# Optimization experiments

Hardware: AMD Instinct MI355X
Metric: run time of the kernel (lower is better)

Reference implementation:

```python
import jax, jax.numpy as jnp
import numpy as np

N_NODES = 50000
N_EDGES = 500000
ATOM_DIM = 128
BOND_DIM = 64
EMB = 128
N_GRAPHS = 256
NUM_LAYER = 2


def _kaiming_uniform(key, fan_out, fan_in):
    # kaiming_uniform_ with nonlinearity='relu': bound = sqrt(6 / fan_in) * sqrt(2)/1 adjustments
    gain = np.sqrt(2.0)
    bound = gain * np.sqrt(3.0 / fan_in)
    return jax.random.uniform(key, (fan_out, fan_in), jnp.float32, -bound, bound)


def setup_inputs() -> dict:
    key = jax.random.key(0)
    ks = jax.random.split(key, 12)
    x = jax.random.normal(ks[0], (N_NODES, ATOM_DIM), jnp.float32)
    edge_attr = jax.random.normal(ks[1], (N_EDGES, BOND_DIM), jnp.float32)
    edge_index = jax.random.randint(ks[2], (2, N_EDGES), 0, N_NODES, jnp.int64)
    batch = jnp.sort(jax.random.randint(ks[3], (N_NODES,), 0, N_GRAPHS, jnp.int64))
    Wa = _kaiming_uniform(ks[4], EMB, ATOM_DIM)
    ba = jnp.zeros((EMB,), jnp.float32)
    Wb = _kaiming_uniform(ks[5], EMB, BOND_DIM)
    bb = jnp.zeros((EMB,), jnp.float32)
    W1 = _kaiming_uniform(ks[6], EMB, EMB)
    b1 = jnp.zeros((EMB,), jnp.float32)
    W2 = _kaiming_uniform(ks[7], EMB // 2, EMB)
    b2 = jnp.zeros((EMB // 2,), jnp.float32)
    W3 = _kaiming_uniform(ks[8], 1, EMB // 2)
    return {"x": x, "edge_attr": edge_attr, "edge_index": edge_index, "batch": batch,
            "Wa": Wa, "ba": ba, "Wb": Wb, "bb": bb,
            "W1": W1, "b1": b1, "W2": W2, "b2": b2, "W3": W3}


def reference(x, edge_attr, edge_index, batch, Wa, ba, Wb, bb, W1, b1, W2, b2, W3):
    src, dst = edge_index[0], edge_index[1]
    # Step 1: embeddings
    node_emb = x @ Wa.T + ba          # [N, EMB]
    edge_emb = edge_attr @ Wb.T + bb  # [E, EMB]
    # Step 2: message passing layers: gather, multiply with edge_emb, scatter-add, residual
    for _ in range(NUM_LAYER):
        msg = node_emb[src] * edge_emb                           # [E, EMB]
        agg = jax.ops.segment_sum(msg, dst, num_segments=N_NODES)  # [N, EMB]
        node_emb = node_emb + agg
    # Step 3: energy MLP (ReLU first, per nn.Sequential)
    h = jax.nn.relu(node_emb)
    h = jax.nn.relu(h @ W1.T + b1)
    h = jax.nn.relu(h @ W2.T + b2)
    node_energy = h @ W3.T            # [N, 1], no bias
    # Step 4: global add pool over graphs
    dg = jax.ops.segment_sum(node_energy, batch, num_segments=N_GRAPHS)  # [G, 1]
    return dg
```

## Files before the change

kernel.cpp:

```cpp
#include <hip/hip_runtime.h>
#include <cstdio>
#include <cstdint>

#define N_NODES 50000
#define N_EDGES 500000
#define EMB 128
#define BOND 64
#define NGRAPH 256
#define NB_SCAN ((N_NODES + 255) / 256)
#define NSTRIP (N_NODES / 16)
#define HSTR 136

typedef short bf16x8 __attribute__((ext_vector_type(8)));
typedef float f32x4  __attribute__((ext_vector_type(4)));

__device__ __forceinline__ unsigned short f2bf(float v){
  unsigned u = __float_as_uint(v);
  unsigned r = (u + 0x7fffu + ((u >> 16) & 1u)) >> 16;
  return (unsigned short)r;
}
__device__ __forceinline__ float bf2f(unsigned short u){
  return __uint_as_float(((unsigned)u) << 16);
}

__global__ void prep_w(const float* __restrict__ Wa, const float* __restrict__ W1,
                       const float* __restrict__ W2, unsigned short* __restrict__ wabf,
                       unsigned short* __restrict__ w1bf, unsigned short* __restrict__ w2bf)
{
  int i = blockIdx.x * 256 + threadIdx.x;
  int i2 = i & 16383;
  int j = i2 & 7, lb = (i2 >> 3) & 63, kc = (i2 >> 9) & 3, tn = i2 >> 11;
  int lm = lb & 15, q = lb >> 4;
  int row = tn * 16 + lm, col = kc * 32 + q * 8 + j;
  if (i < 16384){
    wabf[i] = f2bf(Wa[row * EMB + col]);
  } else if (i < 32768){
    w1bf[i2] = f2bf(W1[row * EMB + col]);
  } else if (i < 32768 + 8192){
    w2bf[i2] = f2bf(W2[row * EMB + col]);
  }
}

__global__ __launch_bounds__(256) void node_gemm_mfma(const float* __restrict__ x,
    const unsigned short* __restrict__ wabf, const float* __restrict__ ba,
    float* __restrict__ out)
{
  const int t = threadIdx.x;
  const int wv = t >> 6, l = t & 63;
  const int lm = l & 15, q = l >> 4;
  union U8 { bf16x8 v; unsigned short s[8]; };
  const int strip = blockIdx.x * 4 + wv;
  if (strip >= NSTRIP) return;
  const long n0 = (long)strip * 16;

  bf16x8 a[4];
  #pragma unroll
  for (int kc = 0; kc < 4; kc++){
    const float* ap = x + (n0 + lm) * (long)EMB + kc * 32 + q * 8;
    float4 x0 = *(const float4*)ap;
    float4 x1 = *(const float4*)(ap + 4);
    U8 u;
    u.s[0] = f2bf(x0.x); u.s[1] = f2bf(x0.y); u.s[2] = f2bf(x0.z); u.s[3] = f2bf(x0.w);
    u.s[4] = f2bf(x1.x); u.s[5] = f2bf(x1.y); u.s[6] = f2bf(x1.z); u.s[7] = f2bf(x1.w);
    a[kc] = u.v;
  }
  float biasv[8];
  #pragma unroll
  for (int tn = 0; tn < 8; tn++) biasv[tn] = ba[tn * 16 + lm];

  #pragma unroll
  for (int tn = 0; tn < 8; tn++){
    f32x4 acc = {0.f, 0.f, 0.f, 0.f};
    #pragma unroll
    for (int kc = 0; kc < 4; kc++){
      bf16x8 bf = *(const bf16x8*)(wabf + (size_t)((tn * 4 + kc) * 64 + l) * 8);
      acc = __builtin_amdgcn_mfma_f32_16x16x32_bf16(a[kc], bf, acc, 0, 0, 0);
    }
    #pragma unroll
    for (int i = 0; i < 4; i++)
      out[(n0 + q * 4 + i) * (long)EMB + tn * 16 + lm] = acc[i] + biasv[tn];
  }
}

__global__ __launch_bounds__(256) void edge_gemm_mfma(
    const float* __restrict__ attr, const float* __restrict__ Wb,
    const float* __restrict__ bb, const int* __restrict__ cedge,
    unsigned short* __restrict__ eemb)
{
  __shared__ unsigned short hs[4][32 * HSTR];
  const int t = threadIdx.x;
  const int wv = t >> 6;
  const int l  = t & 63;
  const int lm = l & 15;
  const int q  = l >> 4;
  union U8 { bf16x8 v; unsigned short s[8]; };

  bf16x8 bfrag[8][2];
  float bias[8];
  #pragma unroll
  for (int tn = 0; tn < 8; tn++){
    bias[tn] = bb[tn * 16 + lm];
    #pragma unroll
    for (int h = 0; h < 2; h++){
      const float* wp = Wb + (tn * 16 + lm) * BOND + h * 32 + q * 8;
      float4 w0 = *(const float4*)wp;
      float4 w1 = *(const float4*)(wp + 4);
      U8 u;
      u.s[0] = f2bf(w0.x); u.s[1] = f2bf(w0.y); u.s[2] = f2bf(w0.z); u.s[3] = f2bf(w0.w);
      u.s[4] = f2bf(w1.x); u.s[5] = f2bf(w1.y); u.s[6] = f2bf(w1.z); u.s[7] = f2bf(w1.w);
      bfrag[tn][h] = u.v;
    }
  }

  unsigned short* hw = hs[wv];
  const long stride = (long)gridDim.x * 4 * 32;
  for (long p0 = ((long)blockIdx.x * 4 + wv) * 32; p0 < N_EDGES; p0 += stride){
    long eidA = (long)cedge[p0 + lm];
    long eidB = (long)cedge[p0 + 16 + lm];
    bf16x8 afA[2], afB[2];
    #pragma unroll
    for (int h = 0; h < 2; h++){
      const float* apA = attr + eidA * BOND + h * 32 + q * 8;
      const float* apB = attr + eidB * BOND + h * 32 + q * 8;
      float4 a0 = *(const float4*)apA;
      float4 a1 = *(const float4*)(apA + 4);
      float4 b0 = *(const float4*)apB;
      float4 b1 = *(const float4*)(apB + 4);
      U8 u;
      u.s[0] = f2bf(a0.x); u.s[1] = f2bf(a0.y); u.s[2] = f2bf(a0.z); u.s[3] = f2bf(a0.w);
      u.s[4] = f2bf(a1.x); u.s[5] = f2bf(a1.y); u.s[6] = f2bf(a1.z); u.s[7] = f2bf(a1.w);
      afA[h] = u.v;
      u.s[0] = f2bf(b0.x); u.s[1] = f2bf(b0.y); u.s[2] = f2bf(b0.z); u.s[3] = f2bf(b0.w);
      u.s[4] = f2bf(b1.x); u.s[5] = f2bf(b1.y); u.s[6] = f2bf(b1.z); u.s[7] = f2bf(b1.w);
      afB[h] = u.v;
    }
    #pragma unroll
    for (int tn = 0; tn < 8; tn++){
      f32x4 accA = {0.f, 0.f, 0.f, 0.f};
      f32x4 accB = {0.f, 0.f, 0.f, 0.f};
      accA = __builtin_amdgcn_mfma_f32_16x16x32_bf16(afA[0], bfrag[tn][0], accA, 0, 0, 0);
      accA = __builtin_amdgcn_mfma_f32_16x16x32_bf16(afA[1], bfrag[tn][1], accA, 0, 0, 0);
      accB = __builtin_amdgcn_mfma_f32_16x16x32_bf16(afB[0], bfrag[tn][0], accB, 0, 0, 0);
      accB = __builtin_amdgcn_mfma_f32_16x16x32_bf16(afB[1], bfrag[tn][1], accB, 0, 0, 0);
      #pragma unroll
      for (int i = 0; i < 4; i++){
        hw[(q * 4 + i) * HSTR + tn * 16 + lm]        = f2bf(accA[i] + bias[tn]);
        hw[(16 + q * 4 + i) * HSTR + tn * 16 + lm]   = f2bf(accB[i] + bias[tn]);
      }
    }
    #pragma unroll
    for (int rb = 0; rb < 8; rb++){
      int row = rb * 4 + q;
      ushort4 v0 = *(const ushort4*)(hw + row * HSTR + lm * 8);
      ushort4 v1 = *(const ushort4*)(hw + row * HSTR + lm * 8 + 4);
      unsigned short* op = eemb + (p0 + row) * (long)EMB + lm * 8;
      *(ushort4*)op = v0;
      *(ushort4*)(op + 4) = v1;
    }
  }
}


__global__ __launch_bounds__(256) void count_deg(const int* __restrict__ ei,
                                                 int* __restrict__ deg)
{
  int e = blockIdx.x * 256 + threadIdx.x;
  if (e < N_EDGES) atomicAdd(&deg[ei[N_EDGES + e]], 1);
}

__global__ __launch_bounds__(256) void scan_s1(const int* __restrict__ deg,
                                               int* __restrict__ blocksum)
{
  int i = blockIdx.x * 256 + threadIdx.x;
  int lane = threadIdx.x & 63, w = threadIdx.x >> 6;
  int v = (i < N_NODES) ? deg[i] : 0;
  #pragma unroll
  for (int o = 32; o > 0; o >>= 1) v += __shfl_down(v, o, 64);
  __shared__ int ws4[4];
  if (lane == 0) ws4[w] = v;
  __syncthreads();
  if (threadIdx.x == 0) blocksum[blockIdx.x] = ws4[0] + ws4[1] + ws4[2] + ws4[3];
}

__global__ __launch_bounds__(256) void scan_s2(const int* __restrict__ blocksum,
                                               int* __restrict__ blockoff,
                                               int* __restrict__ off)
{
  int t = threadIdx.x;
  int lane = t & 63, w = t >> 6;
  int v = (t < NB_SCAN) ? blocksum[t] : 0;
  int x = v;
  #pragma unroll
  for (int d = 1; d < 64; d <<= 1){
    int y = __shfl_up(x, d, 64);
    if (lane >= d) x += y;
  }
  __shared__ int wsum[4];
  if (lane == 63) wsum[w] = x;
  __syncthreads();
  int wo = 0;
  for (int j = 0; j < w; j++) wo += wsum[j];
  if (t < NB_SCAN) blockoff[t] = wo + x - v;
  if (t == 0) off[N_NODES] = wsum[0] + wsum[1] + wsum[2] + wsum[3];
}

__global__ __launch_bounds__(256) void scan_s3(const int* __restrict__ deg,
    const int* __restrict__ blockoff, int* __restrict__ off, int* __restrict__ fill)
{
  int i = blockIdx.x * 256 + threadIdx.x;
  int lane = threadIdx.x & 63, w = threadIdx.x >> 6;
  int v = (i < N_NODES) ? deg[i] : 0;
  int x = v;
  #pragma unroll
  for (int d = 1; d < 64; d <<= 1){
    int y = __shfl_up(x, d, 64);
    if (lane >= d) x += y;
  }
  __shared__ int wsum[4];
  if (lane == 63) wsum[w] = x;
  __syncthreads();
  int wo = 0;
  for (int j = 0; j < w; j++) wo += wsum[j];
  if (i < N_NODES){
    int excl = blockoff[blockIdx.x] + wo + x - v;
    off[i] = excl;
    fill[i] = excl;
  }
}

__global__ __launch_bounds__(256) void scatter_edges(const int* __restrict__ ei,
    int* __restrict__ fill, int* __restrict__ csrc, int* __restrict__ cedge)
{
  int e = blockIdx.x * 256 + threadIdx.x;
  if (e < N_EDGES){
    int dst = ei[N_EDGES + e];
    int p = atomicAdd(&fill[dst], 1);
    csrc[p] = ei[e];
    cedge[p] = e;
  }
}

__global__ __launch_bounds__(256) void agg_kernel(const float* __restrict__ node_old,
    const unsigned short* __restrict__ eemb, const int* __restrict__ off,
    const int* __restrict__ csrc, float* __restrict__ node_new)
{
  int n = blockIdx.x * 8 + (threadIdx.x >> 5);
  if (n >= N_NODES) return;
  int c0 = (threadIdx.x & 31) * 4;
  int s = off[n], e = off[n + 1];
  float4 accA = *(const float4*)(node_old + (long)n * EMB + c0);
  float4 accB = make_float4(0.f, 0.f, 0.f, 0.f);
  int i = s;
  for (; i + 8 <= e; i += 8){
    int idx[8];
    #pragma unroll
    for (int j = 0; j < 8; j++) idx[j] = csrc[i + j];
    float4 a[8]; ushort4 eb[8];
    #pragma unroll
    for (int j = 0; j < 8; j++){
      a[j]  = *(const float4*)(node_old + (long)idx[j] * EMB + c0);
      eb[j] = *(const ushort4*)(eemb + (long)(i + j) * EMB + c0);
    }
    #pragma unroll
    for (int j = 0; j < 8; j++){
      float4& acc = (j & 1) ? accB : accA;
      acc.x = fmaf(a[j].x, bf2f(eb[j].x), acc.x);
      acc.y = fmaf(a[j].y, bf2f(eb[j].y), acc.y);
      acc.z = fmaf(a[j].z, bf2f(eb[j].z), acc.z);
      acc.w = fmaf(a[j].w, bf2f(eb[j].w), acc.w);
    }
  }
  for (; i < e; i++){
    int src = csrc[i];
    const float4 a = *(const float4*)(node_old + (long)src * EMB + c0);
    ushort4 eb = *(const ushort4*)(eemb + (long)i * EMB + c0);
    accA.x = fmaf(a.x, bf2f(eb.x), accA.x);
    accA.y = fmaf(a.y, bf2f(eb.y), accA.y);
    accA.z = fmaf(a.z, bf2f(eb.z), accA.z);
    accA.w = fmaf(a.w, bf2f(eb.w), accA.w);
  }
  accA.x += accB.x; accA.y += accB.y; accA.z += accB.z; accA.w += accB.w;
  *(float4*)(node_new + (long)n * EMB + c0) = accA;
}

__global__ __launch_bounds__(256) void mlp_mfma_pool(const float* __restrict__ ne,
    const unsigned short* __restrict__ w1bf, const unsigned short* __restrict__ w2bf,
    const float* __restrict__ b1, const float* __restrict__ b2,
    const float* __restrict__ W3, const int* __restrict__ batch,
    float* __restrict__ dg)
{
  __shared__ float h1s[4][16 * 132];
  __shared__ float pool[NGRAPH];
  const int t = threadIdx.x;
  const int wv = t >> 6, l = t & 63;
  const int lm = l & 15, q = l >> 4;
  union U8 { bf16x8 v; unsigned short s[8]; };

  for (int i = t; i < NGRAPH; i += 256) pool[i] = 0.f;
  __syncthreads();

  const int strip = blockIdx.x * 4 + wv;
  if (strip < NSTRIP){
    const long n0 = (long)strip * 16;

    float b1v[8], b2v[4], w3v[4];
    #pragma unroll
    for (int tn = 0; tn < 8; tn++) b1v[tn] = b1[tn * 16 + lm];
    #pragma unroll
    for (int tc = 0; tc < 4; tc++){ b2v[tc] = b2[tc * 16 + lm]; w3v[tc] = W3[tc * 16 + lm]; }

    bf16x8 a1[4];
    #pragma unroll
    for (int kc = 0; kc < 4; kc++){
      const float* ap = ne + (n0 + lm) * (long)EMB + kc * 32 + q * 8;
      float4 x0 = *(const float4*)ap;
      float4 x1 = *(const float4*)(ap + 4);
      U8 u;
      u.s[0] = f2bf(fmaxf(x0.x, 0.f)); u.s[1] = f2bf(fmaxf(x0.y, 0.f));
      u.s[2] = f2bf(fmaxf(x0.z, 0.f)); u.s[3] = f2bf(fmaxf(x0.w, 0.f));
      u.s[4] = f2bf(fmaxf(x1.x, 0.f)); u.s[5] = f2bf(fmaxf(x1.y, 0.f));
      u.s[6] = f2bf(fmaxf(x1.z, 0.f)); u.s[7] = f2bf(fmaxf(x1.w, 0.f));
      a1[kc] = u.v;
    }

    f32x4 acc1[8];
    #pragma unroll
    for (int tn = 0; tn < 8; tn++) acc1[tn] = (f32x4){b1v[tn], b1v[tn], b1v[tn], b1v[tn]};
    #pragma unroll
    for (int kc = 0; kc < 4; kc++){
      #pragma unroll
      for (int tn = 0; tn < 8; tn++){
        bf16x8 bf = *(const bf16x8*)(w1bf + (size_t)((tn * 4 + kc) * 64 + l) * 8);
        acc1[tn] = __builtin_amdgcn_mfma_f32_16x16x32_bf16(a1[kc], bf, acc1[tn], 0, 0, 0);
      }
    }

    float* h1 = h1s[wv];
    #pragma unroll
    for (int tn = 0; tn < 8; tn++)
      #pragma unroll
      for (int i = 0; i < 4; i++)
        h1[(q * 4 + i) * 132 + tn * 16 + lm] = fmaxf(acc1[tn][i], 0.f);
    bf16x8 a2[4];
    #pragma unroll
    for (int kc = 0; kc < 4; kc++){
      const float* hp = h1 + lm * 132 + kc * 32 + q * 8;
      float4 x0 = *(const float4*)hp;
      float4 x1 = *(const float4*)(hp + 4);
      U8 u;
      u.s[0] = f2bf(x0.x); u.s[1] = f2bf(x0.y); u.s[2] = f2bf(x0.z); u.s[3] = f2bf(x0.w);
      u.s[4] = f2bf(x1.x); u.s[5] = f2bf(x1.y); u.s[6] = f2bf(x1.z); u.s[7] = f2bf(x1.w);
      a2[kc] = u.v;
    }

    f32x4 acc2[4];
    #pragma unroll
    for (int tc = 0; tc < 4; tc++) acc2[tc] = (f32x4){b2v[tc], b2v[tc], b2v[tc], b2v[tc]};
    #pragma unroll
    for (int kc = 0; kc < 4; kc++){
      #pragma unroll
      for (int tc = 0; tc < 4; tc++){
        bf16x8 bf = *(const bf16x8*)(w2bf + (size_t)((tc * 4 + kc) * 64 + l) * 8);
        acc2[tc] = __builtin_amdgcn_mfma_f32_16x16x32_bf16(a2[kc], bf, acc2[tc], 0, 0, 0);
      }
    }

    float e4[4];
    #pragma unroll
    for (int i = 0; i < 4; i++){
      float s = 0.f;
      #pragma unroll
      for (int tc = 0; tc < 4; tc++) s = fmaf(fmaxf(acc2[tc][i], 0.f), w3v[tc], s);
      e4[i] = s;
    }
    #pragma unroll
    for (int m = 1; m < 16; m <<= 1)
      #pragma unroll
      for (int i = 0; i < 4; i++) e4[i] += __shfl_xor(e4[i], m, 64);
    if (lm == 0){
      #pragma unroll
      for (int i = 0; i < 4; i++){
        int node = (int)n0 + q * 4 + i;
        atomicAdd(&pool[batch[node]], e4[i]);
      }
    }
  }
  __syncthreads();
  for (int i = t; i < NGRAPH; i += 256){
    float v = pool[i];
    if (v != 0.f) atomicAdd(&dg[i], v);
  }
}

extern "C" void kernel_launch(void* const* d_in, const int* in_sizes, int n_in,
                              void* d_out, int out_size, void* d_ws, size_t ws_size,
                              hipStream_t stream)
{
  const float* x         = (const float*)d_in[0];
  const float* edge_attr = (const float*)d_in[1];
  const int*   ei        = (const int*)d_in[2];
  const int*   batch     = (const int*)d_in[3];
  const float* Wa = (const float*)d_in[4];
  const float* ba = (const float*)d_in[5];
  const float* Wb = (const float*)d_in[6];
  const float* bb = (const float*)d_in[7];
  const float* W1 = (const float*)d_in[8];
  const float* b1 = (const float*)d_in[9];
  const float* W2 = (const float*)d_in[10];
  const float* b2 = (const float*)d_in[11];
  const float* W3 = (const float*)d_in[12];

  char* ws = (char*)d_ws;
  size_t p = 0;
  auto alloc = [&](size_t bytes) -> char* {
    char* q = ws + p;
    p += (bytes + 255) & ~(size_t)255;
    return q;
  };
  float* bufA = (float*)alloc((size_t)N_NODES * EMB * sizeof(float));
  float* bufB = (float*)alloc((size_t)N_NODES * EMB * sizeof(float));
  unsigned short* eemb = (unsigned short*)alloc((size_t)N_EDGES * EMB * 2);
  unsigned short* wabf = (unsigned short*)alloc(16384 * sizeof(short));
  unsigned short* w1bf = (unsigned short*)alloc(16384 * sizeof(short));
  unsigned short* w2bf = (unsigned short*)alloc(8192 * sizeof(short));
  int* deg  = (int*)alloc(N_NODES * sizeof(int));
  int* off  = (int*)alloc((N_NODES + 1) * sizeof(int));
  int* fill = (int*)alloc(N_NODES * sizeof(int));
  int* blocksum = (int*)alloc(NB_SCAN * sizeof(int));
  int* blockoff = (int*)alloc(NB_SCAN * sizeof(int));
  int* csrc  = (int*)alloc((size_t)N_EDGES * sizeof(int));
  int* cedge = (int*)alloc((size_t)N_EDGES * sizeof(int));
  if (p > ws_size){
    fprintf(stderr, "kernel_launch: ws too small (%zu < %zu)\n", ws_size, p);
    return;
  }

  hipMemsetAsync(deg, 0, N_NODES * sizeof(int), stream);
  count_deg<<<(N_EDGES + 255) / 256, 256, 0, stream>>>(ei, deg);
  scan_s1<<<NB_SCAN, 256, 0, stream>>>(deg, blocksum);
  scan_s2<<<1, 256, 0, stream>>>(blocksum, blockoff, off);
  scan_s3<<<NB_SCAN, 256, 0, stream>>>(deg, blockoff, off, fill);
  scatter_edges<<<(N_EDGES + 255) / 256, 256, 0, stream>>>(ei, fill, csrc, cedge);

  prep_w<<<160, 256, 0, stream>>>(Wa, W1, W2, wabf, w1bf, w2bf);
  node_gemm_mfma<<<(NSTRIP + 3) / 4, 256, 0, stream>>>(x, wabf, ba, bufA);
  edge_gemm_mfma<<<1024, 256, 0, stream>>>(edge_attr, Wb, bb, cedge, eemb);

  agg_kernel<<<(N_NODES + 7) / 8, 256, 0, stream>>>(bufA, eemb, off, csrc, bufB);
  agg_kernel<<<(N_NODES + 7) / 8, 256, 0, stream>>>(bufB, eemb, off, csrc, bufA);

  hipMemsetAsync(d_out, 0, NGRAPH * sizeof(float), stream);
  mlp_mfma_pool<<<(NSTRIP + 3) / 4, 256, 0, stream>>>(bufA, w1bf, w2bf, b1, b2, W3, batch, (float*)d_out);
}
```

Measured before the change: 478.4 us.

## Store node embeddings in bf16 and pack CSR src/edge ids into int2

Node embedding buffers change from fp32 to bf16. The node GEMM writes them through a shared-memory staging tile, the aggregation kernels gather and write bf16, and the MLP applies ReLU with a sign-bit mask. This halves the bytes moved by the random gathers in the two message-passing layers. The separate csrc and cedge arrays are merged into one int2 array, and the edge GEMM launch changes from 1024x256 to 2048x128 threads. Rounding the node state to bf16 between layers adds precision loss in the residual accumulation.

```diff
diff --git a/kernel.cpp b/kernel.cpp
--- a/kernel.cpp
+++ b/kernel.cpp
@@ -21,6 +21,9 @@
 }
 __device__ __forceinline__ float bf2f(unsigned short u){
   return __uint_as_float(((unsigned)u) << 16);
+}
+__device__ __forceinline__ unsigned short brelu(unsigned short u){
+  return (u & 0x8000u) ? (unsigned short)0 : u;
 }
 
 __global__ void prep_w(const float* __restrict__ Wa, const float* __restrict__ W1,
@@ -43,8 +46,9 @@
 
 __global__ __launch_bounds__(256) void node_gemm_mfma(const float* __restrict__ x,
     const unsigned short* __restrict__ wabf, const float* __restrict__ ba,
-    float* __restrict__ out)
-{
+    unsigned short* __restrict__ out)
+{
+  __shared__ unsigned short hs[4][16 * HSTR];
   const int t = threadIdx.x;
   const int wv = t >> 6, l = t & 63;
   const int lm = l & 15, q = l >> 4;
@@ -68,6 +72,7 @@
   #pragma unroll
   for (int tn = 0; tn < 8; tn++) biasv[tn] = ba[tn * 16 + lm];
 
+  unsigned short* hw = hs[wv];
   #pragma unroll
   for (int tn = 0; tn < 8; tn++){
     f32x4 acc = {0.f, 0.f, 0.f, 0.f};
@@ -78,16 +83,25 @@
     }
     #pragma unroll
     for (int i = 0; i < 4; i++)
-      out[(n0 + q * 4 + i) * (long)EMB + tn * 16 + lm] = acc[i] + biasv[tn];
-  }
-}
-
-__global__ __launch_bounds__(256) void edge_gemm_mfma(
+      hw[(q * 4 + i) * HSTR + tn * 16 + lm] = f2bf(acc[i] + biasv[tn]);
+  }
+  #pragma unroll
+  for (int rb = 0; rb < 4; rb++){
+    int row = rb * 4 + q;
+    ushort4 v0 = *(const ushort4*)(hw + row * HSTR + lm * 8);
+    ushort4 v1 = *(const ushort4*)(hw + row * HSTR + lm * 8 + 4);
+    unsigned short* op = out + (n0 + row) * (long)EMB + lm * 8;
+    *(ushort4*)op = v0;
+    *(ushort4*)(op + 4) = v1;
+  }
+}
+
+__global__ __launch_bounds__(128) void edge_gemm_mfma(
     const float* __restrict__ attr, const float* __restrict__ Wb,
-    const float* __restrict__ bb, const int* __restrict__ cedge,
+    const float* __restrict__ bb, const int2* __restrict__ cse,
     unsigned short* __restrict__ eemb)
 {
-  __shared__ unsigned short hs[4][32 * HSTR];
+  __shared__ unsigned short hs[2][32 * HSTR];
   const int t = threadIdx.x;
   const int wv = t >> 6;
   const int l  = t & 63;
@@ -113,10 +127,10 @@
   }
 
   unsigned short* hw = hs[wv];
-  const long stride = (long)gridDim.x * 4 * 32;
-  for (long p0 = ((long)blockIdx.x * 4 + wv) * 32; p0 < N_EDGES; p0 += stride){
-    long eidA = (long)cedge[p0 + lm];
-    long eidB = (long)cedge[p0 + 16 + lm];
+  const long stride = (long)gridDim.x * 2 * 32;
+  for (long p0 = ((long)blockIdx.x * 2 + wv) * 32; p0 < N_EDGES; p0 += stride){
+    long eidA = (long)cse[p0 + lm].y;
+    long eidB = (long)cse[p0 + 16 + lm].y;
     bf16x8 afA[2], afB[2];
     #pragma unroll
     for (int h = 0; h < 2; h++){
@@ -144,8 +158,8 @@
       accB = __builtin_amdgcn_mfma_f32_16x16x32_bf16(afB[1], bfrag[tn][1], accB, 0, 0, 0);
       #pragma unroll
       for (int i = 0; i < 4; i++){
-        hw[(q * 4 + i) * HSTR + tn * 16 + lm]        = f2bf(accA[i] + bias[tn]);
-        hw[(16 + q * 4 + i) * HSTR + tn * 16 + lm]   = f2bf(accB[i] + bias[tn]);
+        hw[(q * 4 + i) * HSTR + tn * 16 + lm]      = f2bf(accA[i] + bias[tn]);
+        hw[(16 + q * 4 + i) * HSTR + tn * 16 + lm] = f2bf(accB[i] + bias[tn]);
       }
     }
     #pragma unroll
@@ -229,61 +243,65 @@
 }
 
 __global__ __launch_bounds__(256) void scatter_edges(const int* __restrict__ ei,
-    int* __restrict__ fill, int* __restrict__ csrc, int* __restrict__ cedge)
+    int* __restrict__ fill, int2* __restrict__ cse)
 {
   int e = blockIdx.x * 256 + threadIdx.x;
   if (e < N_EDGES){
     int dst = ei[N_EDGES + e];
     int p = atomicAdd(&fill[dst], 1);
-    csrc[p] = ei[e];
-    cedge[p] = e;
-  }
-}
-
-__global__ __launch_bounds__(256) void agg_kernel(const float* __restrict__ node_old,
+    cse[p] = make_int2(ei[e], e);
+  }
+}
+
+__global__ __launch_bounds__(256) void agg_kernel(const unsigned short* __restrict__ node_old,
     const unsigned short* __restrict__ eemb, const int* __restrict__ off,
-    const int* __restrict__ csrc, float* __restrict__ node_new)
+    const int2* __restrict__ cse, unsigned short* __restrict__ node_new)
 {
   int n = blockIdx.x * 8 + (threadIdx.x >> 5);
   if (n >= N_NODES) return;
   int c0 = (threadIdx.x & 31) * 4;
   int s = off[n], e = off[n + 1];
-  float4 accA = *(const float4*)(node_old + (long)n * EMB + c0);
+  ushort4 r = *(const ushort4*)(node_old + (long)n * EMB + c0);
+  float4 accA = make_float4(bf2f(r.x), bf2f(r.y), bf2f(r.z), bf2f(r.w));
   float4 accB = make_float4(0.f, 0.f, 0.f, 0.f);
   int i = s;
   for (; i + 8 <= e; i += 8){
     int idx[8];
     #pragma unroll
-    for (int j = 0; j < 8; j++) idx[j] = csrc[i + j];
-    float4 a[8]; ushort4 eb[8];
+    for (int j = 0; j < 8; j++) idx[j] = cse[i + j].x;
+    ushort4 a[8], eb[8];
     #pragma unroll
     for (int j = 0; j < 8; j++){
-      a[j]  = *(const float4*)(node_old + (long)idx[j] * EMB + c0);
+      a[j]  = *(const ushort4*)(node_old + (long)idx[j] * EMB + c0);
       eb[j] = *(const ushort4*)(eemb + (long)(i + j) * EMB + c0);
     }
     #pragma unroll
     for (int j = 0; j < 8; j++){
       float4& acc = (j & 1) ? accB : accA;
-      acc.x = fmaf(a[j].x, bf2f(eb[j].x), acc.x);
-      acc.y = fmaf(a[j].y, bf2f(eb[j].y), acc.y);
-      acc.z = fmaf(a[j].z, bf2f(eb[j].z), acc.z);
-      acc.w = fmaf(a[j].w, bf2f(eb[j].w), acc.w);
+      acc.x = fmaf(bf2f(a[j].x), bf2f(eb[j].x), acc.x);
+      acc.y = fmaf(bf2f(a[j].y), bf2f(eb[j].y), acc.y);
+      acc.z = fmaf(bf2f(a[j].z), bf2f(eb[j].z), acc.z);
+      acc.w = fmaf(bf2f(a[j].w), bf2f(eb[j].w), acc.w);
     }
   }
   for (; i < e; i++){
-    int src = csrc[i];
-    const float4 a = *(const float4*)(node_old + (long)src * EMB + c0);
+    int src = cse[i].x;
+    ushort4 a  = *(const ushort4*)(node_old + (long)src * EMB + c0);
     ushort4 eb = *(const ushort4*)(eemb + (long)i * EMB + c0);
-    accA.x = fmaf(a.x, bf2f(eb.x), accA.x);
-    accA.y = fmaf(a.y, bf2f(eb.y), accA.y);
-    accA.z = fmaf(a.z, bf2f(eb.z), accA.z);
-    accA.w = fmaf(a.w, bf2f(eb.w), accA.w);
-  }
-  accA.x += accB.x; accA.y += accB.y; accA.z += accB.z; accA.w += accB.w;
-  *(float4*)(node_new + (long)n * EMB + c0) = accA;
-}
-
-__global__ __launch_bounds__(256) void mlp_mfma_pool(const float* __restrict__ ne,
+    accA.x = fmaf(bf2f(a.x), bf2f(eb.x), accA.x);
+    accA.y = fmaf(bf2f(a.y), bf2f(eb.y), accA.y);
+    accA.z = fmaf(bf2f(a.z), bf2f(eb.z), accA.z);
+    accA.w = fmaf(bf2f(a.w), bf2f(eb.w), accA.w);
+  }
+  ushort4 o;
+  o.x = f2bf(accA.x + accB.x);
+  o.y = f2bf(accA.y + accB.y);
+  o.z = f2bf(accA.z + accB.z);
+  o.w = f2bf(accA.w + accB.w);
+  *(ushort4*)(node_new + (long)n * EMB + c0) = o;
+}
+
+__global__ __launch_bounds__(256) void mlp_mfma_pool(const unsigned short* __restrict__ ne,
     const unsigned short* __restrict__ w1bf, const unsigned short* __restrict__ w2bf,
     const float* __restrict__ b1, const float* __restrict__ b2,
     const float* __restrict__ W3, const int* __restrict__ batch,
@@ -312,14 +330,12 @@
     bf16x8 a1[4];
     #pragma unroll
     for (int kc = 0; kc < 4; kc++){
-      const float* ap = ne + (n0 + lm) * (long)EMB + kc * 32 + q * 8;
-      float4 x0 = *(const float4*)ap;
-      float4 x1 = *(const float4*)(ap + 4);
+      const unsigned short* ap = ne + (n0 + lm) * (long)EMB + kc * 32 + q * 8;
+      ushort4 v0 = *(const ushort4*)ap;
+      ushort4 v1 = *(const ushort4*)(ap + 4);
       U8 u;
-      u.s[0] = f2bf(fmaxf(x0.x, 0.f)); u.s[1] = f2bf(fmaxf(x0.y, 0.f));
-      u.s[2] = f2bf(fmaxf(x0.z, 0.f)); u.s[3] = f2bf(fmaxf(x0.w, 0.f));
-      u.s[4] = f2bf(fmaxf(x1.x, 0.f)); u.s[5] = f2bf(fmaxf(x1.y, 0.f));
-      u.s[6] = f2bf(fmaxf(x1.z, 0.f)); u.s[7] = f2bf(fmaxf(x1.w, 0.f));
+      u.s[0] = brelu(v0.x); u.s[1] = brelu(v0.y); u.s[2] = brelu(v0.z); u.s[3] = brelu(v0.w);
+      u.s[4] = brelu(v1.x); u.s[5] = brelu(v1.y); u.s[6] = brelu(v1.z); u.s[7] = brelu(v1.w);
       a1[kc] = u.v;
     }
 
@@ -417,8 +433,8 @@
     p += (bytes + 255) & ~(size_t)255;
     return q;
   };
-  float* bufA = (float*)alloc((size_t)N_NODES * EMB * sizeof(float));
-  float* bufB = (float*)alloc((size_t)N_NODES * EMB * sizeof(float));
+  unsigned short* bufA = (unsigned short*)alloc((size_t)N_NODES * EMB * 2);
+  unsigned short* bufB = (unsigned short*)alloc((size_t)N_NODES * EMB * 2);
   unsigned short* eemb = (unsigned short*)alloc((size_t)N_EDGES * EMB * 2);
   unsigned short* wabf = (unsigned short*)alloc(16384 * sizeof(short));
   unsigned short* w1bf = (unsigned short*)alloc(16384 * sizeof(short));
@@ -428,8 +444,7 @@
   int* fill = (int*)alloc(N_NODES * sizeof(int));
   int* blocksum = (int*)alloc(NB_SCAN * sizeof(int));
   int* blockoff = (int*)alloc(NB_SCAN * sizeof(int));
-  int* csrc  = (int*)alloc((size_t)N_EDGES * sizeof(int));
-  int* cedge = (int*)alloc((size_t)N_EDGES * sizeof(int));
+  int2* cse = (int2*)alloc((size_t)N_EDGES * sizeof(int2));
   if (p > ws_size){
     fprintf(stderr, "kernel_launch: ws too small (%zu < %zu)\n", ws_size, p);
     return;
@@ -440,14 +455,14 @@
   scan_s1<<<NB_SCAN, 256, 0, stream>>>(deg, blocksum);
   scan_s2<<<1, 256, 0, stream>>>(blocksum, blockoff, off);
   scan_s3<<<NB_SCAN, 256, 0, stream>>>(deg, blockoff, off, fill);
-  scatter_edges<<<(N_EDGES + 255) / 256, 256, 0, stream>>>(ei, fill, csrc, cedge);
+  scatter_edges<<<(N_EDGES + 255) / 256, 256, 0, stream>>>(ei, fill, cse);
 
   prep_w<<<160, 256, 0, stream>>>(Wa, W1, W2, wabf, w1bf, w2bf);
   node_gemm_mfma<<<(NSTRIP + 3) / 4, 256, 0, stream>>>(x, wabf, ba, bufA);
-  edge_gemm_mfma<<<1024, 256, 0, stream>>>(edge_attr, Wb, bb, cedge, eemb);
-
-  agg_kernel<<<(N_NODES + 7) / 8, 256, 0, stream>>>(bufA, eemb, off, csrc, bufB);
-  agg_kernel<<<(N_NODES + 7) / 8, 256, 0, stream>>>(bufB, eemb, off, csrc, bufA);
+  edge_gemm_mfma<<<2048, 128, 0, stream>>>(edge_attr, Wb, bb, cse, eemb);
+
+  agg_kernel<<<(N_NODES + 7) / 8, 256, 0, stream>>>(bufA, eemb, off, cse, bufB);
+  agg_kernel<<<(N_NODES + 7) / 8, 256, 0, stream>>>(bufB, eemb, off, cse, bufA);
 
   hipMemsetAsync(d_out, 0, NGRAPH * sizeof(float), stream);
   mlp_mfma_pool<<<(NSTRIP + 3) / 4, 256, 0, stream>>>(bufA, w1bf, w2bf, b1, b2, W3, batch, (float*)d_out);
```

New measurement: 431.7 us. 9.8% less time.
